# Performance work log

Hardware: AMD Instinct MI355X
Metric: run time of the kernel (lower is better)

Reference implementation:

```python
import jax, jax.numpy as jnp
import numpy as np

B, D_IN, EXPERT_DIM, N_EXPERT, N_TASK = 16384, 1024, 256, 8, 4


def setup_inputs() -> dict:
    key = jax.random.key(0)
    k1, k2, k3 = jax.random.split(key, 3)
    x = jax.random.normal(k1, (B, D_IN), dtype=jnp.float32)
    # Glorot-ish scaling for weights
    We = jax.random.normal(k2, (N_EXPERT, D_IN, EXPERT_DIM), dtype=jnp.float32) * (1.0 / np.sqrt(D_IN))
    be = jnp.zeros((N_EXPERT, EXPERT_DIM), dtype=jnp.float32)
    Wg = jax.random.normal(k3, (N_TASK, D_IN, N_EXPERT), dtype=jnp.float32) * (1.0 / np.sqrt(D_IN))
    bg = jnp.zeros((N_TASK, N_EXPERT), dtype=jnp.float32)
    return {"x": x, "We": We, "be": be, "Wg": Wg, "bg": bg}


def reference(x, We, be, Wg, bg):
    # Experts: grouped GEMM -> [B, n_expert, expert_dim]
    E = jax.nn.relu(jnp.einsum("bd,edh->beh", x, We) + be[None, :, :])
    # Gates: [B, n_task, n_expert], softmax over experts
    G = jax.nn.softmax(jnp.einsum("bd,tde->bte", x, Wg) + bg[None, :, :], axis=-1)
    # Gated combine per task: towers[t] = E^T @ g_t -> [n_task, B, expert_dim]
    towers = jnp.einsum("beh,bte->tbh", E, G)
    return towers  # stacked version of the original list of [B, expert_dim] towers
```

## Files before the change

### kernel.cpp

```cpp
#include <hip/hip_runtime.h>

#define B_ROWS 16384
#define D_IN   1024
#define H_DIM  256
#define N_EXP  8
#define N_TASK 4
#define NKT    16

typedef short bf16x8 __attribute__((ext_vector_type(8)));
typedef float f32x4  __attribute__((ext_vector_type(4)));
typedef unsigned short u16x8 __attribute__((ext_vector_type(8)));

static __device__ __forceinline__ unsigned short f2bf(float f) {
  unsigned int u = __float_as_uint(f);
  u += 0x7fffu + ((u >> 16) & 1u);
  return (unsigned short)(u >> 16);
}

#define WS_XB   0u
#define WS_WET  33554432u
#define WS_WGT  37748736u
#define WS_GT   37814272u

__global__ void k_prep_w(const float* __restrict__ We, const float* __restrict__ Wg,
                         unsigned short* __restrict__ We_t, unsigned short* __restrict__ Wg_t) {
  int bid = blockIdx.x;
  int t = threadIdx.x;
  if (bid < 512) {
    int e = bid >> 6;
    int tl = bid & 63;
    int k0 = (tl >> 2) * 64, h0 = (tl & 3) * 64;
    __shared__ unsigned short tile[64][72];
    const float* src = We + (size_t)e * (D_IN * H_DIM);
#pragma unroll
    for (int i = 0; i < 4; ++i) {
      int kk = (t >> 4) + i * 16;
      int hh = (t & 15) * 4;
      float4 v = *(const float4*)(src + (size_t)(k0 + kk) * H_DIM + h0 + hh);
      tile[hh + 0][kk] = f2bf(v.x);
      tile[hh + 1][kk] = f2bf(v.y);
      tile[hh + 2][kk] = f2bf(v.z);
      tile[hh + 3][kk] = f2bf(v.w);
    }
    __syncthreads();
    unsigned short* dst = We_t + (size_t)e * (H_DIM * D_IN);
#pragma unroll
    for (int i = 0; i < 4; ++i) {
      int hh = (t >> 4) + i * 16;
      int kk = (t & 15) * 4;
      ushort4 u = *(const ushort4*)&tile[hh][kk];
      *(ushort4*)(dst + (size_t)(h0 + hh) * D_IN + k0 + kk) = u;
    }
  } else {
    int n = bid - 512;
    int tsk = n >> 3, e = n & 7;
    int k = t * 4;
    const float* src = Wg + (size_t)tsk * (D_IN * 8) + e;
    ushort4 u;
    u.x = f2bf(src[(size_t)(k + 0) * 8]);
    u.y = f2bf(src[(size_t)(k + 1) * 8]);
    u.z = f2bf(src[(size_t)(k + 2) * 8]);
    u.w = f2bf(src[(size_t)(k + 3) * 8]);
    *(ushort4*)(Wg_t + (size_t)n * D_IN + k) = u;
  }
}

__global__ __launch_bounds__(256) void k_gates(const float* __restrict__ x,
                                               const unsigned short* __restrict__ Wg_t,
                                               unsigned short* __restrict__ x_b,
                                               const float* __restrict__ bg,
                                               float* __restrict__ Gt) {
  __shared__ float red[4][16][36];
  int m0 = blockIdx.x * 16;
  int t = threadIdx.x;
  int w = t >> 6, l = t & 63;
  int lr = l & 15, lq = l >> 4;
  int kbase = w * 256;
  f32x4 acc0 = {0.f, 0.f, 0.f, 0.f}, acc1 = {0.f, 0.f, 0.f, 0.f};

  const float* xrow = x + (size_t)(m0 + lr) * D_IN;
  unsigned short* xbrow = x_b + (size_t)(m0 + lr) * D_IN;
  const unsigned short* wg0 = Wg_t + (size_t)lr * D_IN;
  const unsigned short* wg1 = Wg_t + (size_t)(16 + lr) * D_IN;

#pragma unroll
  for (int ks = 0; ks < 8; ++ks) {
    int k = kbase + ks * 32 + lq * 8;
    float4 v0 = *(const float4*)(xrow + k);
    float4 v1 = *(const float4*)(xrow + k + 4);
    bf16x8 a;
    a[0] = (short)f2bf(v0.x); a[1] = (short)f2bf(v0.y);
    a[2] = (short)f2bf(v0.z); a[3] = (short)f2bf(v0.w);
    a[4] = (short)f2bf(v1.x); a[5] = (short)f2bf(v1.y);
    a[6] = (short)f2bf(v1.z); a[7] = (short)f2bf(v1.w);
    *(bf16x8*)(xbrow + k) = a;
    bf16x8 b0 = *(const bf16x8*)(wg0 + k);
    bf16x8 b1 = *(const bf16x8*)(wg1 + k);
    acc0 = __builtin_amdgcn_mfma_f32_16x16x32_bf16(a, b0, acc0, 0, 0, 0);
    acc1 = __builtin_amdgcn_mfma_f32_16x16x32_bf16(a, b1, acc1, 0, 0, 0);
  }

#pragma unroll
  for (int j = 0; j < 4; ++j) {
    red[w][lq * 4 + j][lr]      = acc0[j];
    red[w][lq * 4 + j][16 + lr] = acc1[j];
  }
  __syncthreads();
  if (w == 0) {
#pragma unroll
    for (int j = 0; j < 4; ++j) {
      int rr = lq * 4 + j;
      acc0[j] = red[0][rr][lr] + red[1][rr][lr] + red[2][rr][lr] + red[3][rr][lr];
      acc1[j] = red[0][rr][16 + lr] + red[1][rr][16 + lr] + red[2][rr][16 + lr] + red[3][rr][16 + lr];
    }
    int colb = lr;
    int rbase = m0 + lq * 4;
    float bga = bg[colb], bgb = bg[16 + colb];
#pragma unroll
    for (int j = 0; j < 4; ++j) {
      float va = acc0[j] + bga;
      float vb = acc1[j] + bgb;
      float mxa = va, mxb = vb;
#pragma unroll
      for (int d = 1; d < 8; d <<= 1) {
        mxa = fmaxf(mxa, __shfl_xor(mxa, d));
        mxb = fmaxf(mxb, __shfl_xor(mxb, d));
      }
      va = __expf(va - mxa); vb = __expf(vb - mxb);
      float sa = va, sb = vb;
#pragma unroll
      for (int d = 1; d < 8; d <<= 1) {
        sa += __shfl_xor(sa, d);
        sb += __shfl_xor(sb, d);
      }
      va /= sa; vb /= sb;
      Gt[(size_t)colb * B_ROWS + rbase + j]        = va;
      Gt[(size_t)(16 + colb) * B_ROWS + rbase + j] = vb;
    }
  }
}

__global__ __launch_bounds__(512, 2) void k_expert(const unsigned short* __restrict__ x_b,
                                                   const unsigned short* __restrict__ We_t,
                                                   const float* __restrict__ be,
                                                   const float* __restrict__ Gt,
                                                   float* __restrict__ out) {
  __shared__ unsigned short As[2][256 * 64];
  __shared__ unsigned short Bs[2][256 * 64];
  int bid = blockIdx.x;
  int t = threadIdx.x;

  int xcd = bid & 7;
  int idx = bid >> 3;
  int m   = xcd * 8 + (idx >> 3);
  int hs  = idx & 7;
  int m0  = m * 256;

  int w  = t >> 6, l = t & 63;
  int wm = w >> 2, wn = w & 3;
  int lr = l & 15, lq = l >> 4;

  const unsigned short* Ab = x_b + (size_t)m0 * D_IN;

  const int sr = t >> 3, sg = t & 7;
  const int swz0 = ((lq ^ (lr & 7)) << 3);
  const int swz1 = (((4 + lq) ^ (lr & 7)) << 3);
  const int arow0 = (wm * 128 + lr) << 6;
  const int brow0 = (wn * 64 + lr) << 6;

  size_t bsrc[4];
#pragma unroll
  for (int q2 = 0; q2 < 4; ++q2) {
    int rq = q2 * 64 + sr;
    int me = (rq >> 3) & 7;
    int mh = hs * 32 + ((rq >> 6) & 3) * 8 + (rq & 7);
    bsrc[q2] = (size_t)(me * H_DIM + mh) * D_IN + (size_t)((sg ^ (rq & 7)) << 3);
  }

  f32x4 acc[8][4];
#pragma unroll
  for (int i = 0; i < 8; ++i)
#pragma unroll
    for (int j = 0; j < 4; ++j) acc[i][j] = (f32x4){0.f, 0.f, 0.f, 0.f};

#define STAGE_A(cb, kt, h)                                                                       \
  do {                                                                                           \
    int r0_ = (h) * 128 + sr;                                                                    \
    int r1_ = r0_ + 64;                                                                          \
    __builtin_amdgcn_global_load_lds(                                                            \
        (const __attribute__((address_space(1))) void*)(Ab + (size_t)r0_ * D_IN + (kt) * 64 +    \
                                                        ((sg ^ (r0_ & 7)) << 3)),                \
        (__attribute__((address_space(3))) void*)(&As[(cb)][r0_ * 64 + sg * 8]), 16, 0, 0);      \
    __builtin_amdgcn_global_load_lds(                                                            \
        (const __attribute__((address_space(1))) void*)(Ab + (size_t)r1_ * D_IN + (kt) * 64 +    \
                                                        ((sg ^ (r1_ & 7)) << 3)),                \
        (__attribute__((address_space(3))) void*)(&As[(cb)][r1_ * 64 + sg * 8]), 16, 0, 0);      \
  } while (0)
#define STAGE_B(cb, kt, h)                                                                       \
  do {                                                                                           \
    int r0_ = (h) * 128 + sr;                                                                    \
    int r1_ = r0_ + 64;                                                                          \
    __builtin_amdgcn_global_load_lds(                                                            \
        (const __attribute__((address_space(1))) void*)(We_t + bsrc[2 * (h)] + (kt) * 64),       \
        (__attribute__((address_space(3))) void*)(&Bs[(cb)][r0_ * 64 + sg * 8]), 16, 0, 0);      \
    __builtin_amdgcn_global_load_lds(                                                            \
        (const __attribute__((address_space(1))) void*)(We_t + bsrc[2 * (h) + 1] + (kt) * 64),   \
        (__attribute__((address_space(3))) void*)(&Bs[(cb)][r1_ * 64 + sg * 8]), 16, 0, 0);      \
  } while (0)

  STAGE_A(0, 0, 0); STAGE_A(0, 0, 1);
  STAGE_B(0, 0, 0); STAGE_B(0, 0, 1);
  STAGE_B(1, 1, 0); STAGE_B(1, 1, 1);
  asm volatile("s_waitcnt vmcnt(4)" ::: "memory");
  __builtin_amdgcn_s_barrier();

#pragma unroll 2
  for (int kt = 0; kt < NKT; ++kt) {
    int c = kt & 1;
    const unsigned short* Ap = &As[c][0];
    const unsigned short* Bp = &Bs[c][0];
    bf16x8 b0[4], b1[4];
#pragma unroll
    for (int q = 0; q < 4; ++q) {
      if (q == 0) {
#pragma unroll
        for (int fn = 0; fn < 4; ++fn) {
          b0[fn] = *(const bf16x8*)(Bp + brow0 + fn * 1024 + swz0);
          b1[fn] = *(const bf16x8*)(Bp + brow0 + fn * 1024 + swz1);
        }
      }
      bf16x8 a00 = *(const bf16x8*)(Ap + arow0 + (2 * q) * 1024 + swz0);
      bf16x8 a01 = *(const bf16x8*)(Ap + arow0 + (2 * q) * 1024 + swz1);
      bf16x8 a10 = *(const bf16x8*)(Ap + arow0 + (2 * q + 1) * 1024 + swz0);
      bf16x8 a11 = *(const bf16x8*)(Ap + arow0 + (2 * q + 1) * 1024 + swz1);
      if (q == 0)      { if (kt + 1 < NKT) STAGE_A(c ^ 1, kt + 1, 0); }
      else if (q == 1) { if (kt + 1 < NKT) STAGE_A(c ^ 1, kt + 1, 1); }
      else if (q == 2) { if (kt + 2 < NKT) STAGE_B(c, kt + 2, 0); }
      else             { if (kt + 2 < NKT) STAGE_B(c, kt + 2, 1); }
      __builtin_amdgcn_s_barrier();
      asm volatile("s_waitcnt lgkmcnt(0)" ::: "memory");
      __builtin_amdgcn_s_setprio(1);
#pragma unroll
      for (int fn = 0; fn < 4; ++fn) {
        acc[2 * q][fn]     = __builtin_amdgcn_mfma_f32_16x16x32_bf16(a00, b0[fn], acc[2 * q][fn], 0, 0, 0);
        acc[2 * q][fn]     = __builtin_amdgcn_mfma_f32_16x16x32_bf16(a01, b1[fn], acc[2 * q][fn], 0, 0, 0);
        acc[2 * q + 1][fn] = __builtin_amdgcn_mfma_f32_16x16x32_bf16(a10, b0[fn], acc[2 * q + 1][fn], 0, 0, 0);
        acc[2 * q + 1][fn] = __builtin_amdgcn_mfma_f32_16x16x32_bf16(a11, b1[fn], acc[2 * q + 1][fn], 0, 0, 0);
      }
      __builtin_amdgcn_s_setprio(0);
      if (q == 3) {
        if (kt < NKT - 2)        asm volatile("s_waitcnt vmcnt(4)" ::: "memory");
        else if (kt == NKT - 2)  asm volatile("s_waitcnt vmcnt(0)" ::: "memory");
      }
      __builtin_amdgcn_s_barrier();
    }
  }
#undef STAGE_A
#undef STAGE_B

  float (*Gl)[260] = (float (*)[260])(&As[0][0]);
  {
    int n  = t >> 4;
    int c0 = (t & 15) * 16;
    const float* gsrc = Gt + (size_t)n * B_ROWS + m0 + c0;
    f32x4 g0 = *(const f32x4*)(gsrc + 0);
    f32x4 g1 = *(const f32x4*)(gsrc + 4);
    f32x4 g2 = *(const f32x4*)(gsrc + 8);
    f32x4 g3 = *(const f32x4*)(gsrc + 12);
    *(f32x4*)&Gl[n][c0 + 0]  = g0;
    *(f32x4*)&Gl[n][c0 + 4]  = g1;
    *(f32x4*)&Gl[n][c0 + 8]  = g2;
    *(f32x4*)&Gl[n][c0 + 12] = g3;
  }
  __syncthreads();

  int hi = lr >> 3, h7 = lr & 7;
  int hglob = hs * 32 + wn * 8 + h7;
  float bev[4];
#pragma unroll
  for (int fn = 0; fn < 4; ++fn)
    bev[fn] = be[(2 * fn + hi) * H_DIM + hglob];
#pragma unroll
  for (int fm = 0; fm < 8; ++fm) {
    int rloc = wm * 128 + fm * 16 + lq * 4;
    int r0 = m0 + rloc;
    float vv[4][4];
#pragma unroll
    for (int fn = 0; fn < 4; ++fn)
#pragma unroll
      for (int j = 0; j < 4; ++j)
        vv[fn][j] = fmaxf(acc[fm][fn][j] + bev[fn], 0.f);
    float p[4][4];
#pragma unroll
    for (int tk = 0; tk < 4; ++tk) {
      f32x4 gv[4];
#pragma unroll
      for (int fn = 0; fn < 4; ++fn)
        gv[fn] = *(const f32x4*)&Gl[tk * 8 + 2 * fn + hi][rloc];
#pragma unroll
      for (int j = 0; j < 4; ++j)
        p[tk][j] = gv[0][j] * vv[0][j] + gv[1][j] * vv[1][j] +
                   gv[2][j] * vv[2][j] + gv[3][j] * vv[3][j];
    }
#pragma unroll
    for (int j = 0; j < 4; ++j) {
      float sa = hi ? p[0][j] : p[2][j];
      float sb = hi ? p[1][j] : p[3][j];
      float ra = __shfl_xor(sa, 8);
      float rb = __shfl_xor(sb, 8);
      float t0 = (hi ? p[2][j] : p[0][j]) + ra;
      float t1 = (hi ? p[3][j] : p[1][j]) + rb;
      size_t tk0 = (size_t)(hi * 2);
      out[(tk0 * B_ROWS + r0 + j) * H_DIM + hglob]       = t0;
      out[((tk0 + 1) * B_ROWS + r0 + j) * H_DIM + hglob] = t1;
    }
  }
}

extern "C" void kernel_launch(void* const* d_in, const int* in_sizes, int n_in,
                              void* d_out, int out_size, void* d_ws, size_t ws_size,
                              hipStream_t stream) {
  const float* x  = (const float*)d_in[0];
  const float* We = (const float*)d_in[1];
  const float* be = (const float*)d_in[2];
  const float* Wg = (const float*)d_in[3];
  const float* bg = (const float*)d_in[4];
  float* out = (float*)d_out;
  char* ws = (char*)d_ws;
  unsigned short* x_b  = (unsigned short*)(ws + WS_XB);
  unsigned short* We_t = (unsigned short*)(ws + WS_WET);
  unsigned short* Wg_t = (unsigned short*)(ws + WS_WGT);
  float*          Gt   = (float*)(ws + WS_GT);

  k_prep_w<<<544, 256, 0, stream>>>(We, Wg, We_t, Wg_t);
  k_gates<<<B_ROWS / 16, 256, 0, stream>>>(x, Wg_t, x_b, bg, Gt);
  k_expert<<<512, 512, 0, stream>>>(x_b, We_t, be, Gt, out);
}
```

Baseline: 204.2 us.

## Fuse weight prep and gate kernel into one launch, staging gate weights in LDS

Merges the weight-conversion kernel and the gating kernel into a single launch. The first 512 blocks transpose and convert the expert weights, and the remaining 1024 blocks compute gates. Each gate block now converts the full gate weight matrix into LDS itself instead of reading a pre-transposed bf16 copy from global memory. This removes one launch and the dependency between the two kernels, but every gate block redundantly reads and converts 128KB of Wg. The 75KB LDS allocation per block also limits occupancy.

```diff
diff --git a/kernel.cpp b/kernel.cpp
--- a/kernel.cpp
+++ b/kernel.cpp
@@ -19,18 +19,24 @@
 
 #define WS_XB   0u
 #define WS_WET  33554432u
-#define WS_WGT  37748736u
 #define WS_GT   37814272u
 
-__global__ void k_prep_w(const float* __restrict__ We, const float* __restrict__ Wg,
-                         unsigned short* __restrict__ We_t, unsigned short* __restrict__ Wg_t) {
+__global__ __launch_bounds__(256) void k_prep_gates(const float* __restrict__ x,
+                                                    const float* __restrict__ We,
+                                                    const float* __restrict__ Wg,
+                                                    unsigned short* __restrict__ x_b,
+                                                    unsigned short* __restrict__ We_t,
+                                                    const float* __restrict__ bg,
+                                                    float* __restrict__ Gt) {
+  __shared__ char smem[75264];
   int bid = blockIdx.x;
   int t = threadIdx.x;
+
   if (bid < 512) {
+    unsigned short (*tile)[72] = (unsigned short (*)[72])smem;
     int e = bid >> 6;
     int tl = bid & 63;
     int k0 = (tl >> 2) * 64, h0 = (tl & 3) * 64;
-    __shared__ unsigned short tile[64][72];
     const float* src = We + (size_t)e * (D_IN * H_DIM);
 #pragma unroll
     for (int i = 0; i < 4; ++i) {
@@ -51,28 +57,26 @@
       ushort4 u = *(const ushort4*)&tile[hh][kk];
       *(ushort4*)(dst + (size_t)(h0 + hh) * D_IN + k0 + kk) = u;
     }
-  } else {
-    int n = bid - 512;
-    int tsk = n >> 3, e = n & 7;
-    int k = t * 4;
-    const float* src = Wg + (size_t)tsk * (D_IN * 8) + e;
-    ushort4 u;
-    u.x = f2bf(src[(size_t)(k + 0) * 8]);
-    u.y = f2bf(src[(size_t)(k + 1) * 8]);
-    u.z = f2bf(src[(size_t)(k + 2) * 8]);
-    u.w = f2bf(src[(size_t)(k + 3) * 8]);
-    *(ushort4*)(Wg_t + (size_t)n * D_IN + k) = u;
-  }
-}
-
-__global__ __launch_bounds__(256) void k_gates(const float* __restrict__ x,
-                                               const unsigned short* __restrict__ Wg_t,
-                                               unsigned short* __restrict__ x_b,
-                                               const float* __restrict__ bg,
-                                               float* __restrict__ Gt) {
-  __shared__ float red[4][16][36];
-  int m0 = blockIdx.x * 16;
-  int t = threadIdx.x;
+    return;
+  }
+
+  unsigned short* wgs = (unsigned short*)smem;
+  float (*red)[16][36] = (float (*)[16][36])(smem + 66048);
+  int m0 = (bid - 512) * 16;
+
+#pragma unroll
+  for (int i = 0; i < 32; ++i) {
+    int idx = t * 4 + i * 1024;
+    float4 v = *(const float4*)(Wg + idx);
+    int kk = (idx >> 3) & 1023;
+    int nb = ((idx >> 13) << 3) + (idx & 7);
+    wgs[(size_t)(nb + 0) * 1032 + kk] = f2bf(v.x);
+    wgs[(size_t)(nb + 1) * 1032 + kk] = f2bf(v.y);
+    wgs[(size_t)(nb + 2) * 1032 + kk] = f2bf(v.z);
+    wgs[(size_t)(nb + 3) * 1032 + kk] = f2bf(v.w);
+  }
+  __syncthreads();
+
   int w = t >> 6, l = t & 63;
   int lr = l & 15, lq = l >> 4;
   int kbase = w * 256;
@@ -80,8 +84,8 @@
 
   const float* xrow = x + (size_t)(m0 + lr) * D_IN;
   unsigned short* xbrow = x_b + (size_t)(m0 + lr) * D_IN;
-  const unsigned short* wg0 = Wg_t + (size_t)lr * D_IN;
-  const unsigned short* wg1 = Wg_t + (size_t)(16 + lr) * D_IN;
+  const unsigned short* wg0 = wgs + (size_t)lr * 1032;
+  const unsigned short* wg1 = wgs + (size_t)(16 + lr) * 1032;
 
 #pragma unroll
   for (int ks = 0; ks < 8; ++ks) {
@@ -329,10 +333,8 @@
   char* ws = (char*)d_ws;
   unsigned short* x_b  = (unsigned short*)(ws + WS_XB);
   unsigned short* We_t = (unsigned short*)(ws + WS_WET);
-  unsigned short* Wg_t = (unsigned short*)(ws + WS_WGT);
   float*          Gt   = (float*)(ws + WS_GT);
 
-  k_prep_w<<<544, 256, 0, stream>>>(We, Wg, We_t, Wg_t);
-  k_gates<<<B_ROWS / 16, 256, 0, stream>>>(x, Wg_t, x_b, bg, Gt);
+  k_prep_gates<<<1536, 256, 0, stream>>>(x, We, Wg, x_b, We_t, bg, Gt);
   k_expert<<<512, 512, 0, stream>>>(x_b, We_t, be, Gt, out);
 }
```

Result: faster. 199.1 us (-2.5%).
